# Performance work log

Measured on AMD Instinct MI355X. Metric: run time of the kernel, lower is better.

Reference implementation:

```python
import jax, jax.numpy as jnp
import numpy as np


def setup_inputs() -> dict:
    key = jax.random.key(0)
    k1, k2, k3, k4 = jax.random.split(key, 4)
    B, T, L, C, F = 1024, 128, 256, 2, 784
    x = jax.random.normal(k1, (B, T, F), dtype=jnp.float32)
    W = jax.random.normal(k2, (L, F), dtype=jnp.float32) * (1.0 / np.sqrt(F))
    b = jax.random.normal(k3, (L,), dtype=jnp.float32) * 0.01
    contribution = jax.random.normal(k4, (T, L, C), dtype=jnp.float32)
    return {"x": x, "W": W, "b": b, "contribution": contribution}


def reference(x, W, b, contribution):
    # symbolic_paths: Linear(784 -> leaf) + Hardtanh  -> [B, T, L]
    sp = jnp.clip(jnp.einsum('btf,lf->btl', x, W) + b, -1.0, 1.0)
    # per-(tree,leaf) outer product: class_value[b,t,l,c] = sp[b,t,l] * contribution[t,l,c]
    cv = sp[..., None] * contribution[None]          # [B, T, L, C]
    p = jax.nn.softmax(cv, axis=-1)                  # softmax over classes
    gini = jnp.sum(1.0 - p * p, axis=-1)             # [B, T, L]
    return (sp, gini)
```

## Files before the change

kernel.cpp:

```cpp
#include <hip/hip_runtime.h>
#include <hip/hip_bf16.h>

typedef __attribute__((ext_vector_type(8))) short bf16x8;
typedef __attribute__((ext_vector_type(4))) float f32x4;

#define B_SZ   1024
#define T_SZ   128
#define L_SZ   256
#define F_SZ   784
#define M_TOT  (B_SZ * T_SZ)
#define BM     128
#define BK     32
#define KSTEPS 25

#define WPRE_ELEMS (KSTEPS * 4 * L_SZ)
#define WPRE_BYTES (WPRE_ELEMS * 16)
#define CDIFF_ELEMS (T_SZ * L_SZ)
#define WS_NEED (WPRE_BYTES + CDIFF_ELEMS * 4)

__device__ __forceinline__ unsigned short f2bf(float f) {
    __hip_bfloat16 h = __float2bfloat16(f);
    return *reinterpret_cast<unsigned short*>(&h);
}

#define GLD16(g, l)                                                          \
    __builtin_amdgcn_global_load_lds(                                        \
        (const __attribute__((address_space(1))) void*)(g),                  \
        (__attribute__((address_space(3))) void*)(l), 16, 0, 0)

__global__ __launch_bounds__(256) void dn_prep(
    const float* __restrict__ W, const float* __restrict__ contrib,
    unsigned short* __restrict__ wpre, float* __restrict__ cdiff)
{
    const int gid = blockIdx.x * 256 + threadIdx.x;
    if (gid < WPRE_ELEMS) {
        const int leaf = gid & 255;
        const int kg   = (gid >> 8) & 3;
        const int ks   = gid >> 10;
        const int k0   = ks * BK + kg * 8;
        bf16x8 v;
        #pragma unroll
        for (int j = 0; j < 8; ++j) {
            const int k = k0 + j;
            const float f = (k < F_SZ) ? W[(size_t)leaf * F_SZ + k] : 0.f;
            v[j] = (short)f2bf(f);
        }
        *reinterpret_cast<bf16x8*>(wpre + (size_t)gid * 8) = v;
    } else {
        const int cid = gid - WPRE_ELEMS;
        if (cid < CDIFF_ELEMS)
            cdiff[cid] = contrib[(size_t)cid * 2] - contrib[(size_t)cid * 2 + 1];
    }
}

__global__ __launch_bounds__(512) void dn_fused2(
    const float* __restrict__ x, const unsigned short* __restrict__ wpre,
    const float* __restrict__ bias, const float* __restrict__ cdiff,
    float* __restrict__ out)
{
    __shared__ bf16x8 As[2][4][BM];
    __shared__ bf16x8 Bs[2][4][L_SZ];

    const int tid    = threadIdx.x;
    const int lane   = tid & 63;
    const int wid    = tid >> 6;
    const int waveM  = wid >> 2;
    const int waveN  = wid & 3;
    const int blkRow = blockIdx.x * BM;

    const int ar = tid >> 2;
    const int ak = (tid & 3) * 8;

    const int laneRow = lane & 15;
    const int kgrp    = lane >> 4;

    f32x4 acc[4][4];
    #pragma unroll
    for (int i = 0; i < 4; ++i)
        #pragma unroll
        for (int j = 0; j < 4; ++j)
            acc[i][j] = (f32x4){0.f, 0.f, 0.f, 0.f};

    const float* xrow = x + (size_t)(blkRow + ar) * F_SZ;
    const f32x4  zf   = {0.f, 0.f, 0.f, 0.f};
    f32x4 xa0, xa1;

    auto loadx = [&](int p) {
        const int kb = p * BK;
        if (kb + ak < F_SZ) {
            xa0 = *reinterpret_cast<const f32x4*>(xrow + kb + ak);
            xa1 = *reinterpret_cast<const f32x4*>(xrow + kb + ak + 4);
        } else { xa0 = zf; xa1 = zf; }
    };
    auto cvtA = [&](int b) {
        bf16x8 av;
        #pragma unroll
        for (int j = 0; j < 4; ++j) {
            av[j]     = (short)f2bf(xa0[j]);
            av[4 + j] = (short)f2bf(xa1[j]);
        }
        As[b][ak >> 3][ar] = av;
    };
    auto stageB = [&](int b, int p) {
        const char* g = (const char*)wpre + (size_t)p * 16384 + wid * 2048 + lane * 16;
        char*       l = ((char*)&Bs[b][0][0]) + wid * 2048;
        GLD16(g, l);
        GLD16(g + 1024, l + 1024);
    };

    loadx(0);
    cvtA(0);
    stageB(0, 0);
    loadx(1);
    __syncthreads();

    for (int k = 0; k < KSTEPS; ++k) {
        const int cur = k & 1, nxt = cur ^ 1;
        if (k + 1 < KSTEPS) {
            cvtA(nxt);
            stageB(nxt, k + 1);
            if (k + 2 < KSTEPS) loadx(k + 2);
        }

        bf16x8 af[4], bfv[4];
        #pragma unroll
        for (int mi = 0; mi < 4; ++mi)
            af[mi] = As[cur][kgrp][waveM * 64 + mi * 16 + laneRow];
        #pragma unroll
        for (int ni = 0; ni < 4; ++ni)
            bfv[ni] = Bs[cur][kgrp][waveN * 64 + ni * 16 + laneRow];

        __builtin_amdgcn_s_setprio(1);
        #pragma unroll
        for (int mi = 0; mi < 4; ++mi)
            #pragma unroll
            for (int ni = 0; ni < 4; ++ni)
                acc[mi][ni] = __builtin_amdgcn_mfma_f32_16x16x32_bf16(
                    af[mi], bfv[ni], acc[mi][ni], 0, 0, 0);
        __builtin_amdgcn_s_setprio(0);
        __syncthreads();
    }

    const size_t GOFF  = (size_t)M_TOT * L_SZ;
    const int    rbase = waveM * 64 + (lane >> 4) * 4;
    const int    cbase = waveN * 64 + laneRow;
    #pragma unroll
    for (int ni = 0; ni < 4; ++ni) {
        const int col = cbase + ni * 16;
        const float bb = bias[col];
        #pragma unroll
        for (int mi = 0; mi < 4; ++mi) {
            #pragma unroll
            for (int r = 0; r < 4; ++r) {
                const int m = blkRow + rbase + mi * 16 + r;
                const int t = m & (T_SZ - 1);
                float v  = acc[mi][ni][r] + bb;
                float sp = fminf(fmaxf(v, -1.f), 1.f);
                const float d  = sp * cdiff[t * L_SZ + col];
                const float ed = __expf(d);
                const float s  = ed / (1.f + ed);
                const float g  = fmaf(2.f * s, 1.f - s, 1.f);
                const size_t o = (size_t)m * L_SZ + col;
                out[o]        = sp;
                out[GOFF + o] = g;
            }
        }
    }
}

__global__ __launch_bounds__(512) void dn_fused_v1(
    const float* __restrict__ x, const float* __restrict__ W,
    const float* __restrict__ bias, const float* __restrict__ contrib,
    float* __restrict__ out)
{
    __shared__ bf16x8 As[4][BM];
    __shared__ bf16x8 Bs[4][L_SZ];

    const int tid    = threadIdx.x;
    const int lane   = tid & 63;
    const int wid    = tid >> 6;
    const int waveM  = wid >> 2;
    const int waveN  = wid & 3;
    const int blkRow = blockIdx.x * BM;
    const int ar = tid >> 2;
    const int ak = (tid & 3) * 8;
    const int wr = tid >> 1;
    const int wk = (tid & 1) * 16;
    const int laneRow = lane & 15;
    const int kgrp    = lane >> 4;

    f32x4 acc[4][4];
    #pragma unroll
    for (int i = 0; i < 4; ++i)
        #pragma unroll
        for (int j = 0; j < 4; ++j)
            acc[i][j] = (f32x4){0.f, 0.f, 0.f, 0.f};

    const float* xrow = x + (size_t)(blkRow + ar) * F_SZ;
    const float* wrow = W + (size_t)wr * F_SZ;
    const f32x4 zf = {0.f, 0.f, 0.f, 0.f};

    f32x4 xa0 = *reinterpret_cast<const f32x4*>(xrow + ak);
    f32x4 xa1 = *reinterpret_cast<const f32x4*>(xrow + ak + 4);
    f32x4 wa0 = *reinterpret_cast<const f32x4*>(wrow + wk);
    f32x4 wa1 = *reinterpret_cast<const f32x4*>(wrow + wk + 4);
    f32x4 wa2 = *reinterpret_cast<const f32x4*>(wrow + wk + 8);
    f32x4 wa3 = *reinterpret_cast<const f32x4*>(wrow + wk + 12);

    for (int ks = 0; ks < KSTEPS; ++ks) {
        bf16x8 av, wv0, wv1;
        #pragma unroll
        for (int j = 0; j < 4; ++j) {
            av[j]      = (short)f2bf(xa0[j]);
            av[4 + j]  = (short)f2bf(xa1[j]);
            wv0[j]     = (short)f2bf(wa0[j]);
            wv0[4 + j] = (short)f2bf(wa1[j]);
            wv1[j]     = (short)f2bf(wa2[j]);
            wv1[4 + j] = (short)f2bf(wa3[j]);
        }
        As[ak >> 3][ar] = av;
        Bs[wk >> 3][wr] = wv0;
        Bs[(wk >> 3) + 1][wr] = wv1;
        __syncthreads();

        if (ks + 1 < KSTEPS) {
            const int kb = (ks + 1) * BK;
            if (kb + ak < F_SZ) {
                xa0 = *reinterpret_cast<const f32x4*>(xrow + kb + ak);
                xa1 = *reinterpret_cast<const f32x4*>(xrow + kb + ak + 4);
            } else { xa0 = zf; xa1 = zf; }
            if (kb + wk < F_SZ) {
                wa0 = *reinterpret_cast<const f32x4*>(wrow + kb + wk);
                wa1 = *reinterpret_cast<const f32x4*>(wrow + kb + wk + 4);
                wa2 = *reinterpret_cast<const f32x4*>(wrow + kb + wk + 8);
                wa3 = *reinterpret_cast<const f32x4*>(wrow + kb + wk + 12);
            } else { wa0 = zf; wa1 = zf; wa2 = zf; wa3 = zf; }
        }

        bf16x8 af[4], bfv[4];
        #pragma unroll
        for (int mi = 0; mi < 4; ++mi)
            af[mi] = As[kgrp][waveM * 64 + mi * 16 + laneRow];
        #pragma unroll
        for (int ni = 0; ni < 4; ++ni)
            bfv[ni] = Bs[kgrp][waveN * 64 + ni * 16 + laneRow];
        #pragma unroll
        for (int mi = 0; mi < 4; ++mi)
            #pragma unroll
            for (int ni = 0; ni < 4; ++ni)
                acc[mi][ni] = __builtin_amdgcn_mfma_f32_16x16x32_bf16(
                    af[mi], bfv[ni], acc[mi][ni], 0, 0, 0);
        __syncthreads();
    }

    const size_t GOFF  = (size_t)M_TOT * L_SZ;
    const int    rbase = waveM * 64 + (lane >> 4) * 4;
    const int    cbase = waveN * 64 + laneRow;
    #pragma unroll
    for (int ni = 0; ni < 4; ++ni) {
        const int col = cbase + ni * 16;
        const float bb = bias[col];
        #pragma unroll
        for (int mi = 0; mi < 4; ++mi) {
            #pragma unroll
            for (int r = 0; r < 4; ++r) {
                const int m = blkRow + rbase + mi * 16 + r;
                const int t = m & (T_SZ - 1);
                float v  = acc[mi][ni][r] + bb;
                float sp = fminf(fmaxf(v, -1.f), 1.f);
                const float* cp = contrib + (size_t)(t * L_SZ + col) * 2;
                const float d  = sp * (cp[0] - cp[1]);
                const float ed = __expf(d);
                const float s  = ed / (1.f + ed);
                const float g  = fmaf(2.f * s, 1.f - s, 1.f);
                const size_t o = (size_t)m * L_SZ + col;
                out[o]        = sp;
                out[GOFF + o] = g;
            }
        }
    }
}

extern "C" void kernel_launch(void* const* d_in, const int* in_sizes, int n_in,
                              void* d_out, int out_size, void* d_ws, size_t ws_size,
                              hipStream_t stream) {
    const float* x       = (const float*)d_in[0];
    const float* W       = (const float*)d_in[1];
    const float* bias    = (const float*)d_in[2];
    const float* contrib = (const float*)d_in[3];
    float* out = (float*)d_out;

    if (ws_size >= (size_t)WS_NEED && d_ws != nullptr) {
        unsigned short* wpre  = (unsigned short*)d_ws;
        float*          cdiff = (float*)((char*)d_ws + WPRE_BYTES);
        const int prep_threads = WPRE_ELEMS + CDIFF_ELEMS;
        dn_prep<<<(prep_threads + 255) / 256, 256, 0, stream>>>(W, contrib, wpre, cdiff);
        dn_fused2<<<M_TOT / BM, 512, 0, stream>>>(x, wpre, bias, cdiff, out);
    } else {
        dn_fused_v1<<<M_TOT / BM, 512, 0, stream>>>(x, W, bias, contrib, out);
    }
}
```

Before: 213.9 us.

## Replace LDS-staged GEMM with register-direct loads and split columns across blocks

The fused GEMM+epilogue kernel drops shared-memory staging and barriers. Each wave now loads its x rows and pre-packed bf16 W fragments straight from global memory into registers and issues MFMAs on them. Blocks are 256 threads with two-per-CU launch bounds, each covering 128 rows by 128 columns, and grouped block ordering so that both column halves of a row group run close together and share x in cache. This removes LDS traffic and synchronisation, but every x row is now fetched twice, W is re-read by every wave, and there is no explicit prefetch pipelining. The last K step loads in-bounds x addresses and relies on the zero-padded W entries to cancel them.

```diff
diff --git a/kernel.cpp b/kernel.cpp
--- a/kernel.cpp
+++ b/kernel.cpp
@@ -9,7 +9,6 @@
 #define L_SZ   256
 #define F_SZ   784
 #define M_TOT  (B_SZ * T_SZ)
-#define BM     128
 #define BK     32
 #define KSTEPS 25
 
@@ -22,11 +21,6 @@
     __hip_bfloat16 h = __float2bfloat16(f);
     return *reinterpret_cast<unsigned short*>(&h);
 }
-
-#define GLD16(g, l)                                                          \
-    __builtin_amdgcn_global_load_lds(                                        \
-        (const __attribute__((address_space(1))) void*)(g),                  \
-        (__attribute__((address_space(3))) void*)(l), 16, 0, 0)
 
 __global__ __launch_bounds__(256) void dn_prep(
     const float* __restrict__ W, const float* __restrict__ contrib,
@@ -53,106 +47,100 @@
     }
 }
 
-__global__ __launch_bounds__(512) void dn_fused2(
+__global__ __launch_bounds__(256, 2) void dn_fused3(
     const float* __restrict__ x, const unsigned short* __restrict__ wpre,
     const float* __restrict__ bias, const float* __restrict__ cdiff,
     float* __restrict__ out)
 {
-    __shared__ bf16x8 As[2][4][BM];
-    __shared__ bf16x8 Bs[2][4][L_SZ];
-
-    const int tid    = threadIdx.x;
-    const int lane   = tid & 63;
-    const int wid    = tid >> 6;
-    const int waveM  = wid >> 2;
-    const int waveN  = wid & 3;
-    const int blkRow = blockIdx.x * BM;
-
-    const int ar = tid >> 2;
-    const int ak = (tid & 3) * 8;
-
-    const int laneRow = lane & 15;
-    const int kgrp    = lane >> 4;
-
-    f32x4 acc[4][4];
-    #pragma unroll
-    for (int i = 0; i < 4; ++i)
-        #pragma unroll
-        for (int j = 0; j < 4; ++j)
-            acc[i][j] = (f32x4){0.f, 0.f, 0.f, 0.f};
-
-    const float* xrow = x + (size_t)(blkRow + ar) * F_SZ;
-    const f32x4  zf   = {0.f, 0.f, 0.f, 0.f};
-    f32x4 xa0, xa1;
-
-    auto loadx = [&](int p) {
-        const int kb = p * BK;
-        if (kb + ak < F_SZ) {
-            xa0 = *reinterpret_cast<const f32x4*>(xrow + kb + ak);
-            xa1 = *reinterpret_cast<const f32x4*>(xrow + kb + ak + 4);
-        } else { xa0 = zf; xa1 = zf; }
-    };
-    auto cvtA = [&](int b) {
-        bf16x8 av;
+    const int tid  = threadIdx.x;
+    const int lane = tid & 63;
+    const int wid  = tid >> 6;
+    const int lr   = lane & 15;
+    const int kseg = lane >> 4;
+
+    const int bid      = blockIdx.x;
+    const int rowGroup = ((bid >> 4) << 3) | (bid & 7);
+    const int colHalf  = (bid >> 3) & 1;
+    const int rowBase  = rowGroup * 128 + wid * 32;
+    const int colBase  = colHalf * 128;
+
+    const float* xp0 = x + (size_t)(rowBase + lr) * F_SZ + kseg * 8;
+    const float* xp1 = xp0 + (size_t)16 * F_SZ;
+    const unsigned short* wp = wpre + ((size_t)kseg * L_SZ + colBase + lr) * 8;
+
+    f32x4 acc[2][8];
+    #pragma unroll
+    for (int mi = 0; mi < 2; ++mi)
+        #pragma unroll
+        for (int ni = 0; ni < 8; ++ni)
+            acc[mi][ni] = (f32x4){0.f, 0.f, 0.f, 0.f};
+
+    #pragma unroll
+    for (int ks = 0; ks < 24; ++ks) {
+        const f32x4 a00 = *reinterpret_cast<const f32x4*>(xp0 + ks * 32);
+        const f32x4 a01 = *reinterpret_cast<const f32x4*>(xp0 + ks * 32 + 4);
+        const f32x4 a10 = *reinterpret_cast<const f32x4*>(xp1 + ks * 32);
+        const f32x4 a11 = *reinterpret_cast<const f32x4*>(xp1 + ks * 32 + 4);
+
+        bf16x8 bv[8];
+        #pragma unroll
+        for (int ni = 0; ni < 8; ++ni)
+            bv[ni] = *reinterpret_cast<const bf16x8*>(wp + (size_t)ks * 8192 + ni * 128);
+
+        bf16x8 a0, a1;
         #pragma unroll
         for (int j = 0; j < 4; ++j) {
-            av[j]     = (short)f2bf(xa0[j]);
-            av[4 + j] = (short)f2bf(xa1[j]);
-        }
-        As[b][ak >> 3][ar] = av;
-    };
-    auto stageB = [&](int b, int p) {
-        const char* g = (const char*)wpre + (size_t)p * 16384 + wid * 2048 + lane * 16;
-        char*       l = ((char*)&Bs[b][0][0]) + wid * 2048;
-        GLD16(g, l);
-        GLD16(g + 1024, l + 1024);
-    };
-
-    loadx(0);
-    cvtA(0);
-    stageB(0, 0);
-    loadx(1);
-    __syncthreads();
-
-    for (int k = 0; k < KSTEPS; ++k) {
-        const int cur = k & 1, nxt = cur ^ 1;
-        if (k + 1 < KSTEPS) {
-            cvtA(nxt);
-            stageB(nxt, k + 1);
-            if (k + 2 < KSTEPS) loadx(k + 2);
-        }
-
-        bf16x8 af[4], bfv[4];
-        #pragma unroll
-        for (int mi = 0; mi < 4; ++mi)
-            af[mi] = As[cur][kgrp][waveM * 64 + mi * 16 + laneRow];
-        #pragma unroll
-        for (int ni = 0; ni < 4; ++ni)
-            bfv[ni] = Bs[cur][kgrp][waveN * 64 + ni * 16 + laneRow];
-
-        __builtin_amdgcn_s_setprio(1);
-        #pragma unroll
-        for (int mi = 0; mi < 4; ++mi)
-            #pragma unroll
-            for (int ni = 0; ni < 4; ++ni)
-                acc[mi][ni] = __builtin_amdgcn_mfma_f32_16x16x32_bf16(
-                    af[mi], bfv[ni], acc[mi][ni], 0, 0, 0);
-        __builtin_amdgcn_s_setprio(0);
-        __syncthreads();
-    }
-
-    const size_t GOFF  = (size_t)M_TOT * L_SZ;
-    const int    rbase = waveM * 64 + (lane >> 4) * 4;
-    const int    cbase = waveN * 64 + laneRow;
-    #pragma unroll
-    for (int ni = 0; ni < 4; ++ni) {
-        const int col = cbase + ni * 16;
+            a0[j]     = (short)f2bf(a00[j]);
+            a0[4 + j] = (short)f2bf(a01[j]);
+            a1[j]     = (short)f2bf(a10[j]);
+            a1[4 + j] = (short)f2bf(a11[j]);
+        }
+
+        #pragma unroll
+        for (int ni = 0; ni < 8; ++ni) {
+            acc[0][ni] = __builtin_amdgcn_mfma_f32_16x16x32_bf16(a0, bv[ni], acc[0][ni], 0, 0, 0);
+            acc[1][ni] = __builtin_amdgcn_mfma_f32_16x16x32_bf16(a1, bv[ni], acc[1][ni], 0, 0, 0);
+        }
+    }
+
+    {
+        const int toff = (kseg < 2) ? 768 : -(kseg * 8);
+        const f32x4 a00 = *reinterpret_cast<const f32x4*>(xp0 + toff);
+        const f32x4 a01 = *reinterpret_cast<const f32x4*>(xp0 + toff + 4);
+        const f32x4 a10 = *reinterpret_cast<const f32x4*>(xp1 + toff);
+        const f32x4 a11 = *reinterpret_cast<const f32x4*>(xp1 + toff + 4);
+
+        bf16x8 bv[8];
+        #pragma unroll
+        for (int ni = 0; ni < 8; ++ni)
+            bv[ni] = *reinterpret_cast<const bf16x8*>(wp + (size_t)24 * 8192 + ni * 128);
+
+        bf16x8 a0, a1;
+        #pragma unroll
+        for (int j = 0; j < 4; ++j) {
+            a0[j]     = (short)f2bf(a00[j]);
+            a0[4 + j] = (short)f2bf(a01[j]);
+            a1[j]     = (short)f2bf(a10[j]);
+            a1[4 + j] = (short)f2bf(a11[j]);
+        }
+
+        #pragma unroll
+        for (int ni = 0; ni < 8; ++ni) {
+            acc[0][ni] = __builtin_amdgcn_mfma_f32_16x16x32_bf16(a0, bv[ni], acc[0][ni], 0, 0, 0);
+            acc[1][ni] = __builtin_amdgcn_mfma_f32_16x16x32_bf16(a1, bv[ni], acc[1][ni], 0, 0, 0);
+        }
+    }
+
+    const size_t GOFF = (size_t)M_TOT * L_SZ;
+    #pragma unroll
+    for (int ni = 0; ni < 8; ++ni) {
+        const int col = colBase + ni * 16 + lr;
         const float bb = bias[col];
         #pragma unroll
-        for (int mi = 0; mi < 4; ++mi) {
+        for (int mi = 0; mi < 2; ++mi) {
             #pragma unroll
             for (int r = 0; r < 4; ++r) {
-                const int m = blkRow + rbase + mi * 16 + r;
+                const int m = rowBase + mi * 16 + kseg * 4 + r;
                 const int t = m & (T_SZ - 1);
                 float v  = acc[mi][ni][r] + bb;
                 float sp = fminf(fmaxf(v, -1.f), 1.f);
@@ -173,7 +161,7 @@
     const float* __restrict__ bias, const float* __restrict__ contrib,
     float* __restrict__ out)
 {
-    __shared__ bf16x8 As[4][BM];
+    __shared__ bf16x8 As[4][128];
     __shared__ bf16x8 Bs[4][L_SZ];
 
     const int tid    = threadIdx.x;
@@ -181,7 +169,7 @@
     const int wid    = tid >> 6;
     const int waveM  = wid >> 2;
     const int waveN  = wid & 3;
-    const int blkRow = blockIdx.x * BM;
+    const int blkRow = blockIdx.x * 128;
     const int ar = tid >> 2;
     const int ak = (tid & 3) * 8;
     const int wr = tid >> 1;
@@ -295,8 +283,8 @@
         float*          cdiff = (float*)((char*)d_ws + WPRE_BYTES);
         const int prep_threads = WPRE_ELEMS + CDIFF_ELEMS;
         dn_prep<<<(prep_threads + 255) / 256, 256, 0, stream>>>(W, contrib, wpre, cdiff);
-        dn_fused2<<<M_TOT / BM, 512, 0, stream>>>(x, wpre, bias, cdiff, out);
+        dn_fused3<<<2048, 256, 0, stream>>>(x, wpre, bias, cdiff, out);
     } else {
-        dn_fused_v1<<<M_TOT / BM, 512, 0, stream>>>(x, W, bias, contrib, out);
-    }
-}
+        dn_fused_v1<<<M_TOT / 128, 512, 0, stream>>>(x, W, bias, contrib, out);
+    }
+}
```

Result: slower. 296.0 us (+38.4%).
